# Kernel optimization log

Hardware: AMD Instinct MI355X
Metric: run time of the kernel (lower is better)

The kernel has to match this reference:

```python
import jax, jax.numpy as jnp
import numpy as np

DEPTH, HEADS, DHEAD, DIM, MLP, RED = 4, 8, 64, 512, 2048, 128
B, P, N = 8, 4, 256


def layer_norm(x, g, b, eps=1e-5):
    m = x.mean(-1, keepdims=True)
    v = ((x - m) ** 2).mean(-1, keepdims=True)
    return (x - m) * jax.lax.rsqrt(v + eps) * g + b


def setup_inputs() -> dict:
    key = jax.random.key(0)
    ks = jax.random.split(key, 24)
    s = 0.02
    inp = {
        "x": jax.random.normal(ks[0], (B, P, N, DIM), jnp.float32),
        # per-layer stacked params (leading axis = depth)
        "ln1_g": jnp.ones((DEPTH, DIM)), "ln1_b": jnp.zeros((DEPTH, DIM)),
        "w_qkv": jax.random.normal(ks[1], (DEPTH, DIM, 3 * HEADS * DHEAD)) * s,
        "w_o": jax.random.normal(ks[2], (DEPTH, HEADS * DHEAD, DIM)) * s,
        "b_o": jnp.zeros((DEPTH, DIM)),
        "ln2_g": jnp.ones((DEPTH, DIM)), "ln2_b": jnp.zeros((DEPTH, DIM)),
        "w1": jax.random.normal(ks[3], (DEPTH, DIM, MLP)) * s, "b1": jnp.zeros((DEPTH, MLP)),
        "w2": jax.random.normal(ks[4], (DEPTH, MLP, DIM)) * s, "b2": jnp.zeros((DEPTH, DIM)),
        # BiAttn params
        "bn_g": jnp.ones((DEPTH, DIM)), "bn_b": jnp.zeros((DEPTH, DIM)),
        "wg": jax.random.normal(ks[5], (DEPTH, DIM, RED)) * s, "bg": jnp.zeros((DEPTH, RED)),
        "wl": jax.random.normal(ks[6], (DEPTH, DIM, RED)) * s, "bl": jnp.zeros((DEPTH, RED)),
        "wc": jax.random.normal(ks[7], (DEPTH, RED, DIM)) * s, "bc": jnp.zeros((DEPTH, DIM)),
        "ws": jax.random.normal(ks[8], (DEPTH, 2 * RED, 1)) * s, "bs": jnp.zeros((DEPTH, 1)),
    }
    return inp


def _attention(x, w_qkv, w_o, b_o):
    b, p, n, _ = x.shape
    qkv = jnp.einsum('bpnd,de->bpne', x, w_qkv)
    q, k, v = jnp.split(qkv, 3, axis=-1)
    def heads(t):
        return t.reshape(b, p, n, HEADS, DHEAD).transpose(0, 1, 3, 2, 4)  # b p h n d
    q, k, v = heads(q), heads(k), heads(v)
    scale = DHEAD ** -0.5
    dots = jnp.einsum('bphnd,bphmd->bphnm', q, k) * scale
    attn = jax.nn.softmax(dots, axis=-1)
    out = jnp.einsum('bphnm,bphmd->bphnd', attn, v)
    out = out.transpose(0, 1, 3, 2, 4).reshape(b, p, n, HEADS * DHEAD)
    return jnp.einsum('bpne,ed->bpnd', out, w_o) + b_o


def _biattn(x, bn_g, bn_b, wg, bg, wl, bl, wc, bc, ws, bs):
    ori = x
    x = layer_norm(x, bn_g, bn_b)
    x_global = x.mean(axis=1, keepdims=True)              # [b,1,n,dim]  (mean over p!)
    x_global = jax.nn.gelu(x_global @ wg + bg, approximate=False)  # [b,1,n,red]
    x_local = jax.nn.gelu(x @ wl + bl, approximate=False)          # [b,p,n,red]
    c_attn = jax.nn.sigmoid(x_global @ wc + bc)           # [b,1,n,dim]
    expand_g = jnp.broadcast_to(x_global, x_local.shape)
    fusion = jnp.concatenate([x_local, expand_g], axis=-1)
    s_attn = jax.nn.sigmoid(fusion @ ws + bs)             # [b,p,n,1]
    return ori * (c_attn * s_attn)


def _mlp(x, w1, b1, w2, b2, bn_g, bn_b, wg, bg, wl, bl, wc, bc, ws, bs):
    h = jax.nn.gelu(x @ w1 + b1, approximate=False)
    h = h @ w2 + b2
    return _biattn(h, bn_g, bn_b, wg, bg, wl, bl, wc, bc, ws, bs)


def reference(x, ln1_g, ln1_b, w_qkv, w_o, b_o, ln2_g, ln2_b, w1, b1, w2, b2,
              bn_g, bn_b, wg, bg, wl, bl, wc, bc, ws, bs):
    for i in range(DEPTH):
        x = _attention(layer_norm(x, ln1_g[i], ln1_b[i]), w_qkv[i], w_o[i], b_o[i]) + x
        x = _mlp(layer_norm(x, ln2_g[i], ln2_b[i]), w1[i], b1[i], w2[i], b2[i],
                 bn_g[i], bn_b[i], wg[i], bg[i], wl[i], bl[i], wc[i], bc[i], ws[i], bs[i]) + x
    return x
```

## Files before the change

kernel.cpp:

```cpp
#include <hip/hip_runtime.h>
#include <hip/hip_bf16.h>
#include <math.h>

typedef __hip_bfloat16 bf16;
typedef unsigned short u16;
typedef __bf16 bf16x8 __attribute__((ext_vector_type(8)));
typedef float f32x4 __attribute__((ext_vector_type(4)));

__device__ __forceinline__ float b2f(bf16 v) { return __bfloat162float(v); }
__device__ __forceinline__ bf16 f2b(float v) { return __float2bfloat16(v); }
__device__ __forceinline__ float bits2f(unsigned int u) {
    union { unsigned int i; float f; } w; w.i = u << 16; return w.f;
}
__device__ __forceinline__ u16 f2bits(float v) {
    union { bf16 h; u16 u; } w; w.h = __float2bfloat16(v); return w.u;
}
__device__ __forceinline__ void async16(void* lds, const void* g) {
    __builtin_amdgcn_global_load_lds(
        (const __attribute__((address_space(1))) unsigned int*)g,
        (__attribute__((address_space(3))) unsigned int*)lds, 16, 0, 0);
}

#define DEPTH 4
#define HEADS 8
#define DHEAD 64
#define DIM 512
#define MLPD 2048
#define RED 128
#define BB 8
#define PP 4
#define NN 256
#define ROWS (BB*PP*NN)
#define XELEMS ((size_t)ROWS*DIM)

__global__ __launch_bounds__(256)
void wtrans_all(const float* __restrict__ W, u16* __restrict__ WT, int K, int N)
{
    __shared__ float T[32][33];
    const int l = blockIdx.z;
    W  += (size_t)l * K * N;
    WT += (size_t)l * N * K;
    const int tx = threadIdx.x & 31, ty = threadIdx.x >> 5;
    const int n0 = blockIdx.x * 32, k0 = blockIdx.y * 32;
#pragma unroll
    for (int r = 0; r < 4; ++r)
        T[ty + r*8][tx] = W[(size_t)(k0 + ty + r*8) * N + n0 + tx];
    __syncthreads();
#pragma unroll
    for (int r = 0; r < 4; ++r)
        WT[(size_t)(n0 + ty + r*8) * K + k0 + tx] = f2bits(T[tx][ty + r*8]);
}

template<int BM, int BN, int BK, int WROWS, int WCOLS>
__global__ __launch_bounds__(256)
void gemm_db(const u16* __restrict__ A, const u16* __restrict__ WT,
             const float* __restrict__ bias, const float* __restrict__ res,
             void* __restrict__ Cv, int M, int N, int K, int act, int outf32)
{
    constexpr int KG  = BK/8;
    constexpr int RPC = 512/BK;
    constexpr int NCA = BM*BK/512;
    constexpr int NCB = BN*BK/512;
    constexpr int CPT = (NCA+NCB)/4;
    constexpr int WM = BM/WROWS, WN = BN/WCOLS;
    constexpr int AM = WM/16, AN = WN/16, KB = BK/32;

    __shared__ u16 As[2][BM*BK];
    __shared__ u16 Bs[2][BN*BK];
    const int tid = threadIdx.x, wave = tid >> 6, lane = tid & 63;
    const int bm = blockIdx.x * BM;
    const int bn = blockIdx.y * BN;
    const int wm = (wave / WCOLS) * WM, wn = (wave % WCOLS) * WN;
    const int lr = lane & 15, quad = lane >> 4;

    const int rowc = lane / KG;
    const int kgs  = ((lane & (KG-1)) ^ (KG == 4 ? ((rowc >> 1) & 3) : (rowc & 7))) * 8;

    auto stage = [&](int buf, int k0) {
#pragma unroll
        for (int t = 0; t < CPT; ++t) {
            const int c = wave*CPT + t;
            if (c < NCA)
                async16(&As[buf][c*512], A  + (size_t)(bm + c*RPC + rowc) * K + k0 + kgs);
            else
                async16(&Bs[buf][(c-NCA)*512], WT + (size_t)(bn + (c-NCA)*RPC + rowc) * K + k0 + kgs);
        }
    };

    f32x4 acc[AM][AN] = {};

    stage(0, 0);
    __syncthreads();

    const int NK = K / BK;
    for (int ki = 0; ki < NK; ++ki) {
        const int cur = ki & 1;
        if (ki + 1 < NK) stage(cur ^ 1, (ki + 1) * BK);

        bf16x8 af[AM][KB], bv[AN][KB];
#pragma unroll
        for (int i = 0; i < AM; ++i) {
            const int rA = wm + i*16 + lr;
            const int sw = (KG == 4 ? (((rA & 15) >> 1) & 3) : (rA & 7));
#pragma unroll
            for (int kb = 0; kb < KB; ++kb)
                af[i][kb] = *(const bf16x8*)(As[cur] + rA*BK + (((kb*4 + quad) ^ sw) * 8));
        }
#pragma unroll
        for (int j = 0; j < AN; ++j) {
            const int rB = wn + j*16 + lr;
            const int sw = (KG == 4 ? (((rB & 15) >> 1) & 3) : (rB & 7));
#pragma unroll
            for (int kb = 0; kb < KB; ++kb)
                bv[j][kb] = *(const bf16x8*)(Bs[cur] + rB*BK + (((kb*4 + quad) ^ sw) * 8));
        }
#pragma unroll
        for (int i = 0; i < AM; ++i)
#pragma unroll
            for (int j = 0; j < AN; ++j)
#pragma unroll
                for (int kb = 0; kb < KB; ++kb)
                    acc[i][j] = __builtin_amdgcn_mfma_f32_16x16x32_bf16(
                        af[i][kb], bv[j][kb], acc[i][j], 0, 0, 0);
        __syncthreads();
    }

#pragma unroll
    for (int i = 0; i < AM; ++i) {
        const int rowb = bm + wm + i*16 + quad*4;
#pragma unroll
        for (int j = 0; j < AN; ++j) {
            const int col = bn + wn + j*16 + lr;
            const float bvs = bias ? bias[col] : 0.f;
#pragma unroll
            for (int r = 0; r < 4; ++r) {
                float v = acc[i][j][r] + bvs;
                if (act == 1) v = 0.5f * v * (1.0f + erff(v * 0.70710678118f));
                else if (act == 2) v = 1.0f / (1.0f + __expf(-v));
                const size_t idx = (size_t)(rowb + r) * N + col;
                if (res) v += res[idx];
                if (outf32) ((float*)Cv)[idx] = v;
                else        ((u16*)Cv)[idx] = f2bits(v);
            }
        }
    }
}

__global__ __launch_bounds__(256)
void attn_mfma(const u16* __restrict__ qkv, u16* __restrict__ out)
{
    __shared__ u16 Kt[64*72];
    __shared__ u16 Vt[64*72];
    __shared__ u16 Pw[4][16*72];
    const int tid = threadIdx.x;
    const int wave = tid >> 6, lane = tid & 63;
    const int lr = lane & 15, quad = lane >> 4;
    const int bp = blockIdx.x >> 5;
    const int h  = (blockIdx.x >> 2) & 7;
    const int qq = blockIdx.x & 3;
    const u16* base = qkv + (size_t)bp * NN * (3*DIM);
    const int qo = h*DHEAD, ko = DIM + h*DHEAD, vo = 2*DIM + h*DHEAD;
    const int m0 = qq*64 + wave*16;

    bf16x8 qf[2];
#pragma unroll
    for (int kb = 0; kb < 2; ++kb)
        qf[kb] = *(const bf16x8*)(base + (size_t)(m0 + lr)*(3*DIM) + qo + kb*32 + quad*8);

    f32x4 o[4] = {};
    float mrow[4], lrow[4];
#pragma unroll
    for (int r = 0; r < 4; ++r) { mrow[r] = -1e30f; lrow[r] = 0.f; }

    const int sr = tid >> 3, sc = tid & 7;

    for (int t = 0; t < 4; ++t) {
        __syncthreads();
#pragma unroll
        for (int half = 0; half < 2; ++half) {
            const int key = half*32 + sr;
            const u16* krow = base + (size_t)(t*64 + key)*(3*DIM);
            uint4 kv = *(const uint4*)(krow + ko + sc*8);
            *(uint4*)(Kt + key*72 + sc*8) = kv;
            uint4 vv = *(const uint4*)(krow + vo + sc*8);
            const int d0 = sc*8;
            Vt[(d0+0)*72 + key] = (u16)(vv.x & 0xffffu);
            Vt[(d0+1)*72 + key] = (u16)(vv.x >> 16);
            Vt[(d0+2)*72 + key] = (u16)(vv.y & 0xffffu);
            Vt[(d0+3)*72 + key] = (u16)(vv.y >> 16);
            Vt[(d0+4)*72 + key] = (u16)(vv.z & 0xffffu);
            Vt[(d0+5)*72 + key] = (u16)(vv.z >> 16);
            Vt[(d0+6)*72 + key] = (u16)(vv.w & 0xffffu);
            Vt[(d0+7)*72 + key] = (u16)(vv.w >> 16);
        }
        __syncthreads();

        f32x4 s[4] = {};
        bf16x8 kf[4][2];
#pragma unroll
        for (int j = 0; j < 4; ++j)
#pragma unroll
            for (int kb = 0; kb < 2; ++kb)
                kf[j][kb] = *(const bf16x8*)(Kt + (j*16 + lr)*72 + kb*32 + quad*8);
#pragma unroll
        for (int j = 0; j < 4; ++j)
#pragma unroll
            for (int kb = 0; kb < 2; ++kb)
                s[j] = __builtin_amdgcn_mfma_f32_16x16x32_bf16(
                    qf[kb], kf[j][kb], s[j], 0, 0, 0);

        float alpha[4];
#pragma unroll
        for (int r = 0; r < 4; ++r) {
#pragma unroll
            for (int j = 0; j < 4; ++j) s[j][r] *= 0.125f;
            float mt = fmaxf(fmaxf(s[0][r], s[1][r]), fmaxf(s[2][r], s[3][r]));
#pragma unroll
            for (int off = 1; off <= 8; off <<= 1) mt = fmaxf(mt, __shfl_xor(mt, off));
            const float mn = fmaxf(mrow[r], mt);
            alpha[r] = __expf(mrow[r] - mn);
            mrow[r] = mn;
            float ssum = 0.f;
#pragma unroll
            for (int j = 0; j < 4; ++j) {
                const float p = __expf(s[j][r] - mn);
                s[j][r] = p; ssum += p;
            }
#pragma unroll
            for (int off = 1; off <= 8; off <<= 1) ssum += __shfl_xor(ssum, off);
            lrow[r] = lrow[r]*alpha[r] + ssum;
        }

#pragma unroll
        for (int j = 0; j < 4; ++j)
#pragma unroll
            for (int r = 0; r < 4; ++r)
                Pw[wave][(quad*4 + r)*72 + j*16 + lr] = f2bits(s[j][r]);
        __syncthreads();

#pragma unroll
        for (int jd = 0; jd < 4; ++jd)
#pragma unroll
            for (int r = 0; r < 4; ++r)
                o[jd][r] *= alpha[r];

        bf16x8 af[2], bv[4][2];
#pragma unroll
        for (int kb = 0; kb < 2; ++kb)
            af[kb] = *(const bf16x8*)(Pw[wave] + lr*72 + kb*32 + quad*8);
#pragma unroll
        for (int jd = 0; jd < 4; ++jd)
#pragma unroll
            for (int kb = 0; kb < 2; ++kb)
                bv[jd][kb] = *(const bf16x8*)(Vt + (jd*16 + lr)*72 + kb*32 + quad*8);
#pragma unroll
        for (int jd = 0; jd < 4; ++jd)
#pragma unroll
            for (int kb = 0; kb < 2; ++kb)
                o[jd] = __builtin_amdgcn_mfma_f32_16x16x32_bf16(
                    af[kb], bv[jd][kb], o[jd], 0, 0, 0);
    }

#pragma unroll
    for (int r = 0; r < 4; ++r) {
        const float inv = 1.0f / lrow[r];
        const size_t rowg = (size_t)bp*NN + m0 + quad*4 + r;
#pragma unroll
        for (int jd = 0; jd < 4; ++jd)
            out[rowg*DIM + h*DHEAD + jd*16 + lr] = f2bits(o[jd][r] * inv);
    }
}

__global__ __launch_bounds__(256)
void ln_kernel(const float* __restrict__ x, const float* __restrict__ g,
               const float* __restrict__ b, u16* __restrict__ y, int rows)
{
    const int wave = threadIdx.x >> 6, lane = threadIdx.x & 63;
    const int row = blockIdx.x * 4 + wave;
    if (row >= rows) return;
    const float4* xr = (const float4*)(x + (size_t)row * DIM);
    float4 v0 = xr[lane], v1 = xr[lane + 64];
    float s  = v0.x+v0.y+v0.z+v0.w + v1.x+v1.y+v1.z+v1.w;
    float s2 = v0.x*v0.x+v0.y*v0.y+v0.z*v0.z+v0.w*v0.w
             + v1.x*v1.x+v1.y*v1.y+v1.z*v1.z+v1.w*v1.w;
#pragma unroll
    for (int off = 32; off; off >>= 1) { s += __shfl_xor(s, off); s2 += __shfl_xor(s2, off); }
    const float mean = s * (1.f/512.f);
    const float var  = s2 * (1.f/512.f) - mean*mean;
    const float rstd = rsqrtf(var + 1e-5f);
    const float4* gp = (const float4*)g; const float4* bp = (const float4*)b;
    float4 g0 = gp[lane], g1 = gp[lane+64], b0 = bp[lane], b1 = bp[lane+64];
    ushort4 o0, o1;
    o0.x = f2bits((v0.x-mean)*rstd*g0.x + b0.x);
    o0.y = f2bits((v0.y-mean)*rstd*g0.y + b0.y);
    o0.z = f2bits((v0.z-mean)*rstd*g0.z + b0.z);
    o0.w = f2bits((v0.w-mean)*rstd*g0.w + b0.w);
    o1.x = f2bits((v1.x-mean)*rstd*g1.x + b1.x);
    o1.y = f2bits((v1.y-mean)*rstd*g1.y + b1.y);
    o1.z = f2bits((v1.z-mean)*rstd*g1.z + b1.z);
    o1.w = f2bits((v1.w-mean)*rstd*g1.w + b1.w);
    ushort4* yr = (ushort4*)(y + (size_t)row * DIM);
    yr[lane] = o0; yr[lane+64] = o1;
}

__global__ __launch_bounds__(256)
void lnmean_kernel(const float* __restrict__ x, const float* __restrict__ g,
                   const float* __restrict__ b, u16* __restrict__ y,
                   u16* __restrict__ G)
{
    __shared__ float T[4][512];
    const int wave = threadIdx.x >> 6, lane = threadIdx.x & 63;
    const int bb = blockIdx.x >> 8, n = blockIdx.x & 255;
    const int row = (bb*PP + wave)*NN + n;
    const float4* xr = (const float4*)(x + (size_t)row * DIM);
    float4 v0 = xr[lane], v1 = xr[lane + 64];
    float s  = v0.x+v0.y+v0.z+v0.w + v1.x+v1.y+v1.z+v1.w;
    float s2 = v0.x*v0.x+v0.y*v0.y+v0.z*v0.z+v0.w*v0.w
             + v1.x*v1.x+v1.y*v1.y+v1.z*v1.z+v1.w*v1.w;
#pragma unroll
    for (int off = 32; off; off >>= 1) { s += __shfl_xor(s, off); s2 += __shfl_xor(s2, off); }
    const float mean = s * (1.f/512.f);
    const float var  = s2 * (1.f/512.f) - mean*mean;
    const float rstd = rsqrtf(var + 1e-5f);
    const float4* gp = (const float4*)g; const float4* bp = (const float4*)b;
    float4 g0 = gp[lane], g1 = gp[lane+64], b0 = bp[lane], b1 = bp[lane+64];
    float4 y0, y1;
    y0.x = (v0.x-mean)*rstd*g0.x + b0.x;
    y0.y = (v0.y-mean)*rstd*g0.y + b0.y;
    y0.z = (v0.z-mean)*rstd*g0.z + b0.z;
    y0.w = (v0.w-mean)*rstd*g0.w + b0.w;
    y1.x = (v1.x-mean)*rstd*g1.x + b1.x;
    y1.y = (v1.y-mean)*rstd*g1.y + b1.y;
    y1.z = (v1.z-mean)*rstd*g1.z + b1.z;
    y1.w = (v1.w-mean)*rstd*g1.w + b1.w;
    ushort4 o0, o1;
    o0.x = f2bits(y0.x); o0.y = f2bits(y0.y); o0.z = f2bits(y0.z); o0.w = f2bits(y0.w);
    o1.x = f2bits(y1.x); o1.y = f2bits(y1.y); o1.z = f2bits(y1.z); o1.w = f2bits(y1.w);
    ushort4* yr = (ushort4*)(y + (size_t)row * DIM);
    yr[lane] = o0; yr[lane+64] = o1;
    *(float4*)&T[wave][lane*4]       = y0;
    *(float4*)&T[wave][256 + lane*4] = y1;
    __syncthreads();
    const int d0 = threadIdx.x;
    const float m0 = (T[0][d0]     + T[1][d0]     + T[2][d0]     + T[3][d0])     * 0.25f;
    const float m1 = (T[0][d0+256] + T[1][d0+256] + T[2][d0+256] + T[3][d0+256]) * 0.25f;
    u16* gr = G + ((size_t)bb*NN + n)*DIM;
    gr[d0]       = f2bits(m0);
    gr[d0 + 256] = f2bits(m1);
}

__global__ __launch_bounds__(256)
void fuse2_kernel(const float4* __restrict__ xb, const float4* __restrict__ m1,
                  const u16* __restrict__ ca, const u16* __restrict__ xl,
                  const u16* __restrict__ xg, const float* __restrict__ wsv,
                  const float* __restrict__ bs, float4* __restrict__ xa)
{
    const int wave = threadIdx.x >> 6, lane = threadIdx.x & 63;
    const int row = blockIdx.x * 4 + wave;
    const int b = row >> 10, n = row & 255;
    const u16* xlr = xl + (size_t)row * RED;
    const u16* xgr = xg + ((size_t)b*NN + n) * RED;
    float s = bits2f(xlr[lane])    * wsv[lane]
            + bits2f(xlr[lane+64]) * wsv[lane+64]
            + bits2f(xgr[lane])    * wsv[RED+lane]
            + bits2f(xgr[lane+64]) * wsv[RED+64+lane];
#pragma unroll
    for (int off = 32; off; off >>= 1) s += __shfl_xor(s, off);
    s = 1.f / (1.f + __expf(-(s + bs[0])));
    const u16* car = ca + ((((size_t)b << 8) + n)*DIM);
#pragma unroll
    for (int t = 0; t < 2; ++t) {
        const int dg = lane + t*64;
        const size_t idx = (size_t)row*128 + dg;
        ushort4 cu = *(const ushort4*)(car + dg*4);
        float4 xv = xb[idx], mv = m1[idx], o;
        o.x = xv.x + mv.x * bits2f(cu.x) * s;
        o.y = xv.y + mv.y * bits2f(cu.y) * s;
        o.z = xv.z + mv.z * bits2f(cu.z) * s;
        o.w = xv.w + mv.w * bits2f(cu.w) * s;
        xa[idx] = o;
    }
}

extern "C" void kernel_launch(void* const* d_in, const int* in_sizes, int n_in,
                              void* d_out, int out_size, void* d_ws, size_t ws_size,
                              hipStream_t stream)
{
    const float* x_in  = (const float*)d_in[0];
    const float* ln1_g = (const float*)d_in[1];
    const float* ln1_b = (const float*)d_in[2];
    const float* w_qkv = (const float*)d_in[3];
    const float* w_o   = (const float*)d_in[4];
    const float* b_o   = (const float*)d_in[5];
    const float* ln2_g = (const float*)d_in[6];
    const float* ln2_b = (const float*)d_in[7];
    const float* w1    = (const float*)d_in[8];
    const float* b1    = (const float*)d_in[9];
    const float* w2    = (const float*)d_in[10];
    const float* b2    = (const float*)d_in[11];
    const float* bn_g  = (const float*)d_in[12];
    const float* bn_b  = (const float*)d_in[13];
    const float* wg    = (const float*)d_in[14];
    const float* bg    = (const float*)d_in[15];
    const float* wl    = (const float*)d_in[16];
    const float* bl    = (const float*)d_in[17];
    const float* wc    = (const float*)d_in[18];
    const float* bc    = (const float*)d_in[19];
    const float* wsw   = (const float*)d_in[20];
    const float* bsb   = (const float*)d_in[21];

    char* ws = (char*)d_ws;
    auto alloc = [&](size_t bytes) {
        char* p = ws;
        ws += (bytes + 255) & ~(size_t)255;
        return p;
    };
    float* XA = (float*)alloc(XELEMS * 4);
    float* XB = (float*)alloc(XELEMS * 4);
    float* M1 = (float*)alloc(XELEMS * 4);
    u16*   L  = (u16*)  alloc(XELEMS * 2);
    u16*   Q  = (u16*)  alloc((size_t)ROWS * 3*DIM * 2);
    u16*   H  = (u16*)  alloc((size_t)ROWS * MLPD * 2);
    u16*   G  = (u16*)  alloc((size_t)BB*NN*DIM * 2);
    u16*   G2 = (u16*)  alloc((size_t)BB*NN*RED * 2);
    u16*   XL = (u16*)  alloc((size_t)ROWS*RED * 2);
    u16*   CA = (u16*)  alloc((size_t)BB*NN*DIM * 2);
    u16* WTqkv = (u16*)alloc((size_t)DEPTH*DIM*3*DIM * 2);
    u16* WTo   = (u16*)alloc((size_t)DEPTH*DIM*DIM * 2);
    u16* WT1   = (u16*)alloc((size_t)DEPTH*DIM*MLPD * 2);
    u16* WT2   = (u16*)alloc((size_t)DEPTH*MLPD*DIM * 2);
    u16* WTl   = (u16*)alloc((size_t)DEPTH*DIM*RED * 2);
    u16* WTg   = (u16*)alloc((size_t)DEPTH*DIM*RED * 2);
    u16* WTc   = (u16*)alloc((size_t)DEPTH*RED*DIM * 2);

    wtrans_all<<<dim3(48,16,DEPTH), 256, 0, stream>>>(w_qkv, WTqkv, DIM, 3*DIM);
    wtrans_all<<<dim3(16,16,DEPTH), 256, 0, stream>>>(w_o,   WTo,   DIM, DIM);
    wtrans_all<<<dim3(64,16,DEPTH), 256, 0, stream>>>(w1,    WT1,   DIM, MLPD);
    wtrans_all<<<dim3(16,64,DEPTH), 256, 0, stream>>>(w2,    WT2,   MLPD, DIM);
    wtrans_all<<<dim3(4,16,DEPTH),  256, 0, stream>>>(wl,    WTl,   DIM, RED);
    wtrans_all<<<dim3(4,16,DEPTH),  256, 0, stream>>>(wg,    WTg,   DIM, RED);
    wtrans_all<<<dim3(16,4,DEPTH),  256, 0, stream>>>(wc,    WTc,   RED, DIM);

    for (int l = 0; l < DEPTH; ++l) {
        const float* Xres = l ? (const float*)XA : x_in;
        ln_kernel<<<ROWS/4, 256, 0, stream>>>(Xres, ln1_g + l*DIM, ln1_b + l*DIM, L, ROWS);
        gemm_db<64,64,64,2,2><<<dim3(128,24), 256, 0, stream>>>(
            L, WTqkv + (size_t)l*DIM*3*DIM, nullptr, nullptr, Q, ROWS, 3*DIM, DIM, 0, 0);
        attn_mfma<<<BB*PP*HEADS*4, 256, 0, stream>>>(Q, L);
        gemm_db<64,64,64,2,2><<<dim3(128,8), 256, 0, stream>>>(
            L, WTo + (size_t)l*DIM*DIM, b_o + l*DIM, Xres, XB, ROWS, DIM, DIM, 0, 1);

        ln_kernel<<<ROWS/4, 256, 0, stream>>>(XB, ln2_g + l*DIM, ln2_b + l*DIM, Q, ROWS);
        gemm_db<64,64,32,2,2><<<dim3(128,32), 256, 0, stream>>>(
            Q, WT1 + (size_t)l*DIM*MLPD, b1 + l*MLPD, nullptr, H, ROWS, MLPD, DIM, 1, 0);
        gemm_db<64,64,64,2,2><<<dim3(128,8), 256, 0, stream>>>(
            H, WT2 + (size_t)l*MLPD*DIM, b2 + l*DIM, nullptr, M1, ROWS, DIM, MLPD, 0, 1);

        lnmean_kernel<<<BB*NN, 256, 0, stream>>>(M1, bn_g + l*DIM, bn_b + l*DIM, L, G);
        gemm_db<64,64,64,2,2><<<dim3(32,2), 256, 0, stream>>>(
            G, WTg + (size_t)l*DIM*RED, bg + l*RED, nullptr, G2, BB*NN, RED, DIM, 1, 0);
        gemm_db<64,64,64,2,2><<<dim3(128,2), 256, 0, stream>>>(
            L, WTl + (size_t)l*DIM*RED, bl + l*RED, nullptr, XL, ROWS, RED, DIM, 1, 0);
        gemm_db<64,64,64,2,2><<<dim3(32,8), 256, 0, stream>>>(
            G2, WTc + (size_t)l*RED*DIM, bc + l*DIM, nullptr, CA, BB*NN, DIM, RED, 2, 0);
        fuse2_kernel<<<ROWS/4, 256, 0, stream>>>((const float4*)XB, (const float4*)M1,
                                                 CA, XL, G2, wsw + (size_t)l*2*RED, bsb + l,
                                                 (l == DEPTH-1) ? (float4*)d_out
                                                                : (float4*)XA);
    }
}
```

Baseline: 904.0 us.

## Fuse weight transposes, merge BiAttn projection GEMMs, fold next-layer LN into fuse2

The seven weight-transpose launches become a single launch that dispatches on block index. The two small BiAttn projections (wl on the local rows, wg on the global mean) now run in one combined GEMM launch with GELU. The next layer's LayerNorm-1 is computed inside fuse2_kernel from the freshly produced residual, which removes one full read pass over the activations and one launch per layer. The folded LayerNorm uses a single-pass E[x^2]-mean^2 variance, which is slightly less numerically robust than a two-pass variance.

```diff
diff --git a/kernel.cpp b/kernel.cpp
--- a/kernel.cpp
+++ b/kernel.cpp
@@ -34,14 +34,28 @@
 #define XELEMS ((size_t)ROWS*DIM)
 
 __global__ __launch_bounds__(256)
-void wtrans_all(const float* __restrict__ W, u16* __restrict__ WT, int K, int N)
+void wtrans_fused(const float* __restrict__ Wqkv, u16* __restrict__ Tqkv,
+                  const float* __restrict__ Wo,   u16* __restrict__ To,
+                  const float* __restrict__ W1,   u16* __restrict__ T1,
+                  const float* __restrict__ W2,   u16* __restrict__ T2,
+                  const float* __restrict__ Wl,   u16* __restrict__ Tl,
+                  const float* __restrict__ Wg,   u16* __restrict__ Tg,
+                  const float* __restrict__ Wc,   u16* __restrict__ Tc)
 {
     __shared__ float T[32][33];
-    const int l = blockIdx.z;
+    const int x = blockIdx.x, l = blockIdx.z;
+    const float* W; u16* WT; int K, N, nx, local;
+    if      (x < 768)  { W=Wqkv; WT=Tqkv; K=512;  N=1536; nx=48; local=x; }
+    else if (x < 1024) { W=Wo;   WT=To;   K=512;  N=512;  nx=16; local=x-768; }
+    else if (x < 2048) { W=W1;   WT=T1;   K=512;  N=2048; nx=64; local=x-1024; }
+    else if (x < 3072) { W=W2;   WT=T2;   K=2048; N=512;  nx=16; local=x-2048; }
+    else if (x < 3136) { W=Wl;   WT=Tl;   K=512;  N=128;  nx=4;  local=x-3072; }
+    else if (x < 3200) { W=Wg;   WT=Tg;   K=512;  N=128;  nx=4;  local=x-3136; }
+    else               { W=Wc;   WT=Tc;   K=128;  N=512;  nx=16; local=x-3200; }
     W  += (size_t)l * K * N;
     WT += (size_t)l * N * K;
+    const int n0 = (local % nx) * 32, k0 = (local / nx) * 32;
     const int tx = threadIdx.x & 31, ty = threadIdx.x >> 5;
-    const int n0 = blockIdx.x * 32, k0 = blockIdx.y * 32;
 #pragma unroll
     for (int r = 0; r < 4; ++r)
         T[ty + r*8][tx] = W[(size_t)(k0 + ty + r*8) * N + n0 + tx];
@@ -141,6 +155,92 @@
                 if (res) v += res[idx];
                 if (outf32) ((float*)Cv)[idx] = v;
                 else        ((u16*)Cv)[idx] = f2bits(v);
+            }
+        }
+    }
+}
+
+__global__ __launch_bounds__(256)
+void gemm_wlg(const u16* __restrict__ L, const u16* __restrict__ G,
+              const u16* __restrict__ WTl, const u16* __restrict__ WTg,
+              const float* __restrict__ bl, const float* __restrict__ bg,
+              u16* __restrict__ XL, u16* __restrict__ G2)
+{
+    constexpr int K = 512, N = 128;
+    const u16* A; const u16* WT; const float* bias; u16* C;
+    int bm, bn;
+    const int blk = blockIdx.x;
+    if (blk < 256) { A = L; WT = WTl; bias = bl; C = XL;
+                     bm = (blk & 127) * 64; bn = (blk >> 7) * 64; }
+    else           { const int b2 = blk - 256; A = G; WT = WTg; bias = bg; C = G2;
+                     bm = (b2 & 31) * 64; bn = (b2 >> 5) * 64; }
+
+    __shared__ u16 As[2][64*64];
+    __shared__ u16 Bs[2][64*64];
+    const int tid = threadIdx.x, wave = tid >> 6, lane = tid & 63;
+    const int wm = (wave >> 1) * 32, wn = (wave & 1) * 32;
+    const int lr = lane & 15, quad = lane >> 4;
+
+    const int rowc = lane >> 3;
+    const int kgs  = ((lane & 7) ^ (rowc & 7)) * 8;
+
+    auto stage = [&](int buf, int k0) {
+#pragma unroll
+        for (int t = 0; t < 4; ++t) {
+            const int c = wave*4 + t;
+            if (c < 8) async16(&As[buf][c*512], A  + (size_t)(bm + c*8 + rowc) * K + k0 + kgs);
+            else       async16(&Bs[buf][(c-8)*512], WT + (size_t)(bn + (c-8)*8 + rowc) * K + k0 + kgs);
+        }
+    };
+
+    f32x4 acc[2][2] = {};
+    stage(0, 0);
+    __syncthreads();
+
+    for (int ki = 0; ki < 8; ++ki) {
+        const int cur = ki & 1;
+        if (ki + 1 < 8) stage(cur ^ 1, (ki + 1) * 64);
+
+        bf16x8 af[2][2], bv[2][2];
+#pragma unroll
+        for (int i = 0; i < 2; ++i) {
+            const int rA = wm + i*16 + lr;
+            const int sw = rA & 7;
+#pragma unroll
+            for (int kb = 0; kb < 2; ++kb)
+                af[i][kb] = *(const bf16x8*)(As[cur] + rA*64 + (((kb*4 + quad) ^ sw) * 8));
+        }
+#pragma unroll
+        for (int j = 0; j < 2; ++j) {
+            const int rB = wn + j*16 + lr;
+            const int sw = rB & 7;
+#pragma unroll
+            for (int kb = 0; kb < 2; ++kb)
+                bv[j][kb] = *(const bf16x8*)(Bs[cur] + rB*64 + (((kb*4 + quad) ^ sw) * 8));
+        }
+#pragma unroll
+        for (int i = 0; i < 2; ++i)
+#pragma unroll
+            for (int j = 0; j < 2; ++j)
+#pragma unroll
+                for (int kb = 0; kb < 2; ++kb)
+                    acc[i][j] = __builtin_amdgcn_mfma_f32_16x16x32_bf16(
+                        af[i][kb], bv[j][kb], acc[i][j], 0, 0, 0);
+        __syncthreads();
+    }
+
+#pragma unroll
+    for (int i = 0; i < 2; ++i) {
+        const int rowb = bm + wm + i*16 + quad*4;
+#pragma unroll
+        for (int j = 0; j < 2; ++j) {
+            const int col = bn + wn + j*16 + lr;
+            const float bvs = bias[col];
+#pragma unroll
+            for (int r = 0; r < 4; ++r) {
+                float v = acc[i][j][r] + bvs;
+                v = 0.5f * v * (1.0f + erff(v * 0.70710678118f));
+                C[(size_t)(rowb + r) * N + col] = f2bits(v);
             }
         }
     }
@@ -353,7 +453,9 @@
 void fuse2_kernel(const float4* __restrict__ xb, const float4* __restrict__ m1,
                   const u16* __restrict__ ca, const u16* __restrict__ xl,
                   const u16* __restrict__ xg, const float* __restrict__ wsv,
-                  const float* __restrict__ bs, float4* __restrict__ xa)
+                  const float* __restrict__ bs, float4* __restrict__ xa,
+                  const float* __restrict__ lng, const float* __restrict__ lnb,
+                  u16* __restrict__ lnout)
 {
     const int wave = threadIdx.x >> 6, lane = threadIdx.x & 63;
     const int row = blockIdx.x * 4 + wave;
@@ -368,17 +470,51 @@
     for (int off = 32; off; off >>= 1) s += __shfl_xor(s, off);
     s = 1.f / (1.f + __expf(-(s + bs[0])));
     const u16* car = ca + ((((size_t)b << 8) + n)*DIM);
-#pragma unroll
-    for (int t = 0; t < 2; ++t) {
-        const int dg = lane + t*64;
-        const size_t idx = (size_t)row*128 + dg;
-        ushort4 cu = *(const ushort4*)(car + dg*4);
-        float4 xv = xb[idx], mv = m1[idx], o;
-        o.x = xv.x + mv.x * bits2f(cu.x) * s;
-        o.y = xv.y + mv.y * bits2f(cu.y) * s;
-        o.z = xv.z + mv.z * bits2f(cu.z) * s;
-        o.w = xv.w + mv.w * bits2f(cu.w) * s;
-        xa[idx] = o;
+
+    float4 o0, o1;
+    {
+        const size_t idx = (size_t)row*128 + lane;
+        ushort4 cu = *(const ushort4*)(car + lane*4);
+        float4 xv = xb[idx], mv = m1[idx];
+        o0.x = xv.x + mv.x * bits2f(cu.x) * s;
+        o0.y = xv.y + mv.y * bits2f(cu.y) * s;
+        o0.z = xv.z + mv.z * bits2f(cu.z) * s;
+        o0.w = xv.w + mv.w * bits2f(cu.w) * s;
+        xa[idx] = o0;
+    }
+    {
+        const size_t idx = (size_t)row*128 + lane + 64;
+        ushort4 cu = *(const ushort4*)(car + (lane + 64)*4);
+        float4 xv = xb[idx], mv = m1[idx];
+        o1.x = xv.x + mv.x * bits2f(cu.x) * s;
+        o1.y = xv.y + mv.y * bits2f(cu.y) * s;
+        o1.z = xv.z + mv.z * bits2f(cu.z) * s;
+        o1.w = xv.w + mv.w * bits2f(cu.w) * s;
+        xa[idx] = o1;
+    }
+
+    if (lnout) {
+        float t  = o0.x+o0.y+o0.z+o0.w + o1.x+o1.y+o1.z+o1.w;
+        float t2 = o0.x*o0.x+o0.y*o0.y+o0.z*o0.z+o0.w*o0.w
+                 + o1.x*o1.x+o1.y*o1.y+o1.z*o1.z+o1.w*o1.w;
+#pragma unroll
+        for (int off = 32; off; off >>= 1) { t += __shfl_xor(t, off); t2 += __shfl_xor(t2, off); }
+        const float mean = t * (1.f/512.f);
+        const float var  = t2 * (1.f/512.f) - mean*mean;
+        const float rstd = rsqrtf(var + 1e-5f);
+        const float4* gp = (const float4*)lng; const float4* bp = (const float4*)lnb;
+        float4 g0 = gp[lane], g1 = gp[lane+64], b0 = bp[lane], b1 = bp[lane+64];
+        ushort4 q0, q1;
+        q0.x = f2bits((o0.x-mean)*rstd*g0.x + b0.x);
+        q0.y = f2bits((o0.y-mean)*rstd*g0.y + b0.y);
+        q0.z = f2bits((o0.z-mean)*rstd*g0.z + b0.z);
+        q0.w = f2bits((o0.w-mean)*rstd*g0.w + b0.w);
+        q1.x = f2bits((o1.x-mean)*rstd*g1.x + b1.x);
+        q1.y = f2bits((o1.y-mean)*rstd*g1.y + b1.y);
+        q1.z = f2bits((o1.z-mean)*rstd*g1.z + b1.z);
+        q1.w = f2bits((o1.w-mean)*rstd*g1.w + b1.w);
+        ushort4* yr = (ushort4*)(lnout + (size_t)row * DIM);
+        yr[lane] = q0; yr[lane+64] = q1;
     }
 }
 
@@ -433,17 +569,13 @@
     u16* WTg   = (u16*)alloc((size_t)DEPTH*DIM*RED * 2);
     u16* WTc   = (u16*)alloc((size_t)DEPTH*RED*DIM * 2);
 
-    wtrans_all<<<dim3(48,16,DEPTH), 256, 0, stream>>>(w_qkv, WTqkv, DIM, 3*DIM);
-    wtrans_all<<<dim3(16,16,DEPTH), 256, 0, stream>>>(w_o,   WTo,   DIM, DIM);
-    wtrans_all<<<dim3(64,16,DEPTH), 256, 0, stream>>>(w1,    WT1,   DIM, MLPD);
-    wtrans_all<<<dim3(16,64,DEPTH), 256, 0, stream>>>(w2,    WT2,   MLPD, DIM);
-    wtrans_all<<<dim3(4,16,DEPTH),  256, 0, stream>>>(wl,    WTl,   DIM, RED);
-    wtrans_all<<<dim3(4,16,DEPTH),  256, 0, stream>>>(wg,    WTg,   DIM, RED);
-    wtrans_all<<<dim3(16,4,DEPTH),  256, 0, stream>>>(wc,    WTc,   RED, DIM);
+    wtrans_fused<<<dim3(3264, 1, DEPTH), 256, 0, stream>>>(
+        w_qkv, WTqkv, w_o, WTo, w1, WT1, w2, WT2, wl, WTl, wg, WTg, wc, WTc);
+
+    ln_kernel<<<ROWS/4, 256, 0, stream>>>(x_in, ln1_g, ln1_b, L, ROWS);
 
     for (int l = 0; l < DEPTH; ++l) {
         const float* Xres = l ? (const float*)XA : x_in;
-        ln_kernel<<<ROWS/4, 256, 0, stream>>>(Xres, ln1_g + l*DIM, ln1_b + l*DIM, L, ROWS);
         gemm_db<64,64,64,2,2><<<dim3(128,24), 256, 0, stream>>>(
             L, WTqkv + (size_t)l*DIM*3*DIM, nullptr, nullptr, Q, ROWS, 3*DIM, DIM, 0, 0);
         attn_mfma<<<BB*PP*HEADS*4, 256, 0, stream>>>(Q, L);
@@ -457,15 +589,17 @@
             H, WT2 + (size_t)l*MLPD*DIM, b2 + l*DIM, nullptr, M1, ROWS, DIM, MLPD, 0, 1);
 
         lnmean_kernel<<<BB*NN, 256, 0, stream>>>(M1, bn_g + l*DIM, bn_b + l*DIM, L, G);
-        gemm_db<64,64,64,2,2><<<dim3(32,2), 256, 0, stream>>>(
-            G, WTg + (size_t)l*DIM*RED, bg + l*RED, nullptr, G2, BB*NN, RED, DIM, 1, 0);
-        gemm_db<64,64,64,2,2><<<dim3(128,2), 256, 0, stream>>>(
-            L, WTl + (size_t)l*DIM*RED, bl + l*RED, nullptr, XL, ROWS, RED, DIM, 1, 0);
+        gemm_wlg<<<320, 256, 0, stream>>>(L, G, WTl + (size_t)l*DIM*RED,
+                                          WTg + (size_t)l*DIM*RED,
+                                          bl + l*RED, bg + l*RED, XL, G2);
         gemm_db<64,64,64,2,2><<<dim3(32,8), 256, 0, stream>>>(
             G2, WTc + (size_t)l*RED*DIM, bc + l*DIM, nullptr, CA, BB*NN, DIM, RED, 2, 0);
-        fuse2_kernel<<<ROWS/4, 256, 0, stream>>>((const float4*)XB, (const float4*)M1,
-                                                 CA, XL, G2, wsw + (size_t)l*2*RED, bsb + l,
-                                                 (l == DEPTH-1) ? (float4*)d_out
-                                                                : (float4*)XA);
-    }
-}
+        const int last = (l == DEPTH-1);
+        fuse2_kernel<<<ROWS/4, 256, 0, stream>>>(
+            (const float4*)XB, (const float4*)M1, CA, XL, G2,
+            wsw + (size_t)l*2*RED, bsb + l,
+            last ? (float4*)d_out : (float4*)XA,
+            ln1_g + (l+1)*DIM, ln1_b + (l+1)*DIM,
+            last ? nullptr : L);
+    }
+}
```

Measured after the change: 836.3 us. -7.5%, faster.
